# Optimization experiments

Hardware: AMD Instinct MI355X
Metric: run time of the kernel (lower is better)

The kernel has to match this reference:

```python
import jax, jax.numpy as jnp
import numpy as np

Q_MAX = 127.0  # int8 symmetric quantization range

def _ste_round(v):
    # straight-through round (matches quantize-forward semantics)
    return v + jax.lax.stop_gradient(jnp.round(v) - v)

def setup_inputs() -> dict:
    key = jax.random.key(0)
    k1, k2, k3, k4 = jax.random.split(key, 4)
    B, S, D_IN, D_OUT = 32, 577, 1024, 2560
    x = jax.random.normal(k1, (B, S, D_IN), dtype=jnp.float32)
    # pre-quantized int8 weight stored as int32 for jax friendliness
    w_int = jax.random.randint(k2, (D_OUT, D_IN), -127, 128, dtype=jnp.int32)
    # per-output-row dequant scales (absmax/127 style, small positive)
    scale_w = jax.random.uniform(k3, (D_OUT,), dtype=jnp.float32, minval=0.005, maxval=0.02)
    bias = jax.random.normal(k4, (D_OUT,), dtype=jnp.float32)
    return {"x": x, "w_int": w_int, "scale_w": scale_w, "bias": bias}

def reference(x, w_int, scale_w, bias):
    # bnb Int8Linear: dynamic per-row int8 quantization of activations,
    # per-column (output-feature) weight scales, then bias add.
    # x: [B, S, D_in], w_int: [D_out, D_in] in [-127,127], scale_w: [D_out]
    absmax_x = jnp.max(jnp.abs(x), axis=-1, keepdims=True)  # [B, S, 1]
    scale_x = jnp.maximum(absmax_x, 1e-8) / Q_MAX
    x_q = _ste_round(x / scale_x)  # quantized activations in [-127, 127]
    # integer-valued GEMM carried in fp32 accumulation
    acc = jnp.einsum("bsd,od->bso", x_q, w_int.astype(jnp.float32))
    y = acc * scale_x * scale_w[None, None, :] + bias[None, None, :]
    return y
```

## Files before the change

### kernel.cpp

```cpp
#include <hip/hip_runtime.h>
#include <stdint.h>

typedef int v4i __attribute__((ext_vector_type(4)));

__device__ __forceinline__ void gll16(const void* g, void* l) {
    __builtin_amdgcn_global_load_lds(
        (const __attribute__((address_space(1))) void*)(uintptr_t)g,
        (__attribute__((address_space(3))) void*)(uint32_t)(uintptr_t)l,
        16, 0, 0);
}

__global__ __launch_bounds__(256) void quant_x(const float* __restrict__ x,
                                               signed char* __restrict__ xq,
                                               float* __restrict__ sx, int M) {
    const int row = blockIdx.x;
    const int tid = threadIdx.x;
    signed char* qrow = xq + (size_t)row * 1024;
    if (row >= M) {
        ((char4*)qrow)[tid] = make_char4(0, 0, 0, 0);
        if (tid == 0) sx[row] = 0.0f;
        return;
    }
    const float4 v = ((const float4*)(x + (size_t)row * 1024))[tid];
    float a = fmaxf(fmaxf(fabsf(v.x), fabsf(v.y)), fmaxf(fabsf(v.z), fabsf(v.w)));
#pragma unroll
    for (int off = 32; off > 0; off >>= 1)
        a = fmaxf(a, __shfl_xor(a, off));
    __shared__ float red[4];
    if ((tid & 63) == 0) red[tid >> 6] = a;
    __syncthreads();
    const float am = fmaxf(fmaxf(red[0], red[1]), fmaxf(red[2], red[3]));
    const float amc = fmaxf(am, 1e-8f);
    const float scale = amc * (1.0f / 127.0f);
    const float inv = 127.0f / amc;
    char4 q;
    q.x = (signed char)(int)rintf(v.x * inv);
    q.y = (signed char)(int)rintf(v.y * inv);
    q.z = (signed char)(int)rintf(v.z * inv);
    q.w = (signed char)(int)rintf(v.w * inv);
    ((char4*)qrow)[tid] = q;
    if (tid == 0) sx[row] = scale;
}

__global__ __launch_bounds__(256) void conv_w(const int* __restrict__ w,
                                              signed char* __restrict__ w8, int n4) {
    const int i = blockIdx.x * 256 + threadIdx.x;
    if (i < n4) {
        const int4 v = ((const int4*)w)[i];
        char4 c;
        c.x = (signed char)v.x; c.y = (signed char)v.y;
        c.z = (signed char)v.z; c.w = (signed char)v.w;
        ((char4*)w8)[i] = c;
    }
}

__global__ __launch_bounds__(256) void gemm_i8(const signed char* __restrict__ xq,
                                               const signed char* __restrict__ w8,
                                               const float* __restrict__ sx,
                                               const float* __restrict__ sw,
                                               const float* __restrict__ bias,
                                               float* __restrict__ out,
                                               int M, int N, int K) {
    __shared__ signed char As[128 * 64];
    __shared__ signed char Bs[128 * 64];

    const int tid  = threadIdx.x;
    const int lane = tid & 63;
    const int wave = tid >> 6;
    const int wm = (wave & 1) * 64;
    const int wn = (wave >> 1) * 64;
    const int m_block = blockIdx.y * 128;
    const int n_block = blockIdx.x * 128;

    v4i acc[4][4];
#pragma unroll
    for (int mt = 0; mt < 4; ++mt)
#pragma unroll
        for (int nt = 0; nt < 4; ++nt) {
            acc[mt][nt].x = 0; acc[mt][nt].y = 0; acc[mt][nt].z = 0; acc[mt][nt].w = 0;
        }

    const int sr = tid >> 2;
    const int sc = ((tid & 3) ^ ((sr >> 1) & 3)) * 16;
    const signed char* aG = xq + (size_t)(m_block + sr) * K + sc;
    const signed char* bG = w8 + (size_t)(n_block + sr) * K + sc;
    signed char* aL = As + wave * 1024;
    signed char* bL = Bs + wave * 1024;

    const int fr  = lane & 15;
    const int fcs = (((lane >> 4) ^ ((lane >> 1) & 3))) * 16;

    for (int k0 = 0; k0 < K; k0 += 64) {
        if (k0) __syncthreads();
        gll16(aG + k0, aL);
        gll16(aG + k0 + (size_t)64 * K, aL + 4096);
        gll16(bG + k0, bL);
        gll16(bG + k0 + (size_t)64 * K, bL + 4096);
        __syncthreads();

        v4i af[4], bf[4];
#pragma unroll
        for (int mt = 0; mt < 4; ++mt)
            af[mt] = *(const v4i*)&As[(wm + mt * 16 + fr) * 64 + fcs];
#pragma unroll
        for (int nt = 0; nt < 4; ++nt)
            bf[nt] = *(const v4i*)&Bs[(wn + nt * 16 + fr) * 64 + fcs];
#pragma unroll
        for (int mt = 0; mt < 4; ++mt)
#pragma unroll
            for (int nt = 0; nt < 4; ++nt)
                acc[mt][nt] = __builtin_amdgcn_mfma_i32_16x16x64_i8(af[mt], bf[nt], acc[mt][nt], 0, 0, 0);
    }

    const int lr = lane >> 4;
    const int lc = lane & 15;
#pragma unroll
    for (int mt = 0; mt < 4; ++mt) {
        const int rbase = m_block + wm + mt * 16 + lr * 4;
        float sxv[4];
#pragma unroll
        for (int r = 0; r < 4; ++r)
            sxv[r] = (rbase + r < M) ? sx[rbase + r] : 0.0f;
#pragma unroll
        for (int nt = 0; nt < 4; ++nt) {
            const int col = n_block + wn + nt * 16 + lc;
            const float swv = sw[col];
            const float bv  = bias[col];
            const int* a = (const int*)&acc[mt][nt];
#pragma unroll
            for (int r = 0; r < 4; ++r) {
                const int row = rbase + r;
                if (row < M)
                    out[(size_t)row * N + col] = (float)a[r] * sxv[r] * swv + bv;
            }
        }
    }
}

extern "C" void kernel_launch(void* const* d_in, const int* in_sizes, int n_in,
                              void* d_out, int out_size, void* d_ws, size_t ws_size,
                              hipStream_t stream) {
    const float* x       = (const float*)d_in[0];
    const int*   w_int   = (const int*)d_in[1];
    const float* scale_w = (const float*)d_in[2];
    const float* bias    = (const float*)d_in[3];
    float* out = (float*)d_out;

    const int D_OUT = in_sizes[2];
    const int D_IN  = in_sizes[1] / D_OUT;
    const int M     = in_sizes[0] / D_IN;
    const int Mpad  = ((M + 127) / 128) * 128;

    signed char* xq = (signed char*)d_ws;
    signed char* w8 = xq + (size_t)Mpad * D_IN;
    float*       sx = (float*)(w8 + (size_t)D_OUT * D_IN);

    quant_x<<<Mpad, 256, 0, stream>>>(x, xq, sx, M);
    const int n4 = D_OUT * D_IN / 4;
    conv_w<<<(n4 + 255) / 256, 256, 0, stream>>>(w_int, w8, n4);
    dim3 grid(D_OUT / 128, Mpad / 128);
    gemm_i8<<<grid, dim3(256, 1, 1), 0, stream>>>(xq, w8, sx, scale_w, bias, out, M, D_OUT, D_IN);
}
```

Before: 317.5 us.

## Use 32x32x32 int8 MFMA with 128-deep K tiles and fuse prep kernels

Switches the GEMM inner loop from 16x16x64 to 32x32x32 int8 MFMA instructions, doubling the K-tile to 128 with a matching 8-way XOR swizzle in LDS. This means fewer barriers per K and better operand reuse per fragment load. The weight conversion and activation quantization kernels are merged into one launch to drop a kernel launch. The cost is twice the LDS per block (32 KB), which may reduce occupancy, and a 16-element accumulator epilogue with strided row stores.

```diff
diff --git a/kernel.cpp b/kernel.cpp
--- a/kernel.cpp
+++ b/kernel.cpp
@@ -1,7 +1,8 @@
 #include <hip/hip_runtime.h>
 #include <stdint.h>
 
-typedef int v4i __attribute__((ext_vector_type(4)));
+typedef int v4i  __attribute__((ext_vector_type(4)));
+typedef int v16i __attribute__((ext_vector_type(16)));
 
 __device__ __forceinline__ void gll16(const void* g, void* l) {
     __builtin_amdgcn_global_load_lds(
@@ -10,18 +11,30 @@
         16, 0, 0);
 }
 
-__global__ __launch_bounds__(256) void quant_x(const float* __restrict__ x,
-                                               signed char* __restrict__ xq,
-                                               float* __restrict__ sx, int M) {
-    const int row = blockIdx.x;
+__global__ __launch_bounds__(256) void prep(const float* __restrict__ x,
+                                            const int* __restrict__ w,
+                                            signed char* __restrict__ xq,
+                                            signed char* __restrict__ w8,
+                                            float* __restrict__ sx,
+                                            int M, int Mpad) {
+    const int b = blockIdx.x;
     const int tid = threadIdx.x;
-    signed char* qrow = xq + (size_t)row * 1024;
-    if (row >= M) {
-        ((char4*)qrow)[tid] = make_char4(0, 0, 0, 0);
-        if (tid == 0) sx[row] = 0.0f;
+    if (b >= Mpad) {
+        const int r = b - Mpad;
+        const int4 v = ((const int4*)(w + (size_t)r * 1024))[tid];
+        char4 c;
+        c.x = (signed char)v.x; c.y = (signed char)v.y;
+        c.z = (signed char)v.z; c.w = (signed char)v.w;
+        ((char4*)(w8 + (size_t)r * 1024))[tid] = c;
         return;
     }
-    const float4 v = ((const float4*)(x + (size_t)row * 1024))[tid];
+    signed char* qrow = xq + (size_t)b * 1024;
+    if (b >= M) {
+        ((char4*)qrow)[tid] = make_char4(0, 0, 0, 0);
+        if (tid == 0) sx[b] = 0.0f;
+        return;
+    }
+    const float4 v = ((const float4*)(x + (size_t)b * 1024))[tid];
     float a = fmaxf(fmaxf(fabsf(v.x), fabsf(v.y)), fmaxf(fabsf(v.z), fabsf(v.w)));
 #pragma unroll
     for (int off = 32; off > 0; off >>= 1)
@@ -31,7 +44,6 @@
     __syncthreads();
     const float am = fmaxf(fmaxf(red[0], red[1]), fmaxf(red[2], red[3]));
     const float amc = fmaxf(am, 1e-8f);
-    const float scale = amc * (1.0f / 127.0f);
     const float inv = 127.0f / amc;
     char4 q;
     q.x = (signed char)(int)rintf(v.x * inv);
@@ -39,19 +51,7 @@
     q.z = (signed char)(int)rintf(v.z * inv);
     q.w = (signed char)(int)rintf(v.w * inv);
     ((char4*)qrow)[tid] = q;
-    if (tid == 0) sx[row] = scale;
-}
-
-__global__ __launch_bounds__(256) void conv_w(const int* __restrict__ w,
-                                              signed char* __restrict__ w8, int n4) {
-    const int i = blockIdx.x * 256 + threadIdx.x;
-    if (i < n4) {
-        const int4 v = ((const int4*)w)[i];
-        char4 c;
-        c.x = (signed char)v.x; c.y = (signed char)v.y;
-        c.z = (signed char)v.z; c.w = (signed char)v.w;
-        ((char4*)w8)[i] = c;
-    }
+    if (tid == 0) sx[b] = amc * (1.0f / 127.0f);
 }
 
 __global__ __launch_bounds__(256) void gemm_i8(const signed char* __restrict__ xq,
@@ -61,8 +61,8 @@
                                                const float* __restrict__ bias,
                                                float* __restrict__ out,
                                                int M, int N, int K) {
-    __shared__ signed char As[128 * 64];
-    __shared__ signed char Bs[128 * 64];
+    __shared__ signed char As[128 * 128];
+    __shared__ signed char Bs[128 * 128];
 
     const int tid  = threadIdx.x;
     const int lane = tid & 63;
@@ -72,66 +72,75 @@
     const int m_block = blockIdx.y * 128;
     const int n_block = blockIdx.x * 128;
 
-    v4i acc[4][4];
+    v16i acc[2][2];
 #pragma unroll
-    for (int mt = 0; mt < 4; ++mt)
+    for (int mt = 0; mt < 2; ++mt)
 #pragma unroll
-        for (int nt = 0; nt < 4; ++nt) {
-            acc[mt][nt].x = 0; acc[mt][nt].y = 0; acc[mt][nt].z = 0; acc[mt][nt].w = 0;
-        }
+        for (int nt = 0; nt < 2; ++nt)
+#pragma unroll
+            for (int r = 0; r < 16; ++r)
+                acc[mt][nt][r] = 0;
 
-    const int sr = tid >> 2;
-    const int sc = ((tid & 3) ^ ((sr >> 1) & 3)) * 16;
-    const signed char* aG = xq + (size_t)(m_block + sr) * K + sc;
-    const signed char* bG = w8 + (size_t)(n_block + sr) * K + sc;
+    const int trow   = tid >> 3;
+    const int tchunk = ((tid & 7) ^ (trow & 7)) * 16;
+    const signed char* aG = xq + (size_t)(m_block + trow) * K + tchunk;
+    const signed char* bG = w8 + (size_t)(n_block + trow) * K + tchunk;
+    const size_t rowstep = (size_t)32 * K;
     signed char* aL = As + wave * 1024;
     signed char* bL = Bs + wave * 1024;
 
-    const int fr  = lane & 15;
-    const int fcs = (((lane >> 4) ^ ((lane >> 1) & 3))) * 16;
+    const int fr = lane & 31;
+    const int fk = lane >> 5;
+    const int fx = lane & 7;
 
-    for (int k0 = 0; k0 < K; k0 += 64) {
+    for (int k0 = 0; k0 < K; k0 += 128) {
         if (k0) __syncthreads();
-        gll16(aG + k0, aL);
-        gll16(aG + k0 + (size_t)64 * K, aL + 4096);
-        gll16(bG + k0, bL);
-        gll16(bG + k0 + (size_t)64 * K, bL + 4096);
+#pragma unroll
+        for (int i = 0; i < 4; ++i) {
+            gll16(aG + k0 + i * rowstep, aL + i * 4096);
+            gll16(bG + k0 + i * rowstep, bL + i * 4096);
+        }
         __syncthreads();
 
-        v4i af[4], bf[4];
 #pragma unroll
-        for (int mt = 0; mt < 4; ++mt)
-            af[mt] = *(const v4i*)&As[(wm + mt * 16 + fr) * 64 + fcs];
+        for (int kk = 0; kk < 4; ++kk) {
+            const int coff = ((kk * 2 + fk) ^ fx) * 16;
+            v4i af[2], bf[2];
 #pragma unroll
-        for (int nt = 0; nt < 4; ++nt)
-            bf[nt] = *(const v4i*)&Bs[(wn + nt * 16 + fr) * 64 + fcs];
+            for (int mt = 0; mt < 2; ++mt)
+                af[mt] = *(const v4i*)&As[(wm + mt * 32 + fr) * 128 + coff];
 #pragma unroll
-        for (int mt = 0; mt < 4; ++mt)
+            for (int nt = 0; nt < 2; ++nt)
+                bf[nt] = *(const v4i*)&Bs[(wn + nt * 32 + fr) * 128 + coff];
 #pragma unroll
-            for (int nt = 0; nt < 4; ++nt)
-                acc[mt][nt] = __builtin_amdgcn_mfma_i32_16x16x64_i8(af[mt], bf[nt], acc[mt][nt], 0, 0, 0);
+            for (int mt = 0; mt < 2; ++mt)
+#pragma unroll
+                for (int nt = 0; nt < 2; ++nt)
+                    acc[mt][nt] = __builtin_amdgcn_mfma_i32_32x32x32_i8(af[mt], bf[nt], acc[mt][nt], 0, 0, 0);
+        }
     }
 
-    const int lr = lane >> 4;
-    const int lc = lane & 15;
+    const int lc = lane & 31;
+    const int lh = (lane >> 5) * 4;
 #pragma unroll
-    for (int mt = 0; mt < 4; ++mt) {
-        const int rbase = m_block + wm + mt * 16 + lr * 4;
-        float sxv[4];
+    for (int mt = 0; mt < 2; ++mt) {
+        const int rbase = m_block + wm + mt * 32 + lh;
+        float sxv[16];
 #pragma unroll
-        for (int r = 0; r < 4; ++r)
-            sxv[r] = (rbase + r < M) ? sx[rbase + r] : 0.0f;
+        for (int r = 0; r < 16; ++r) {
+            const int row = rbase + (r & 3) + 8 * (r >> 2);
+            sxv[r] = (row < M) ? sx[row] : 0.0f;
+        }
 #pragma unroll
-        for (int nt = 0; nt < 4; ++nt) {
-            const int col = n_block + wn + nt * 16 + lc;
-            const float swv = sw[col];
+        for (int nt = 0; nt < 2; ++nt) {
+            const int col = n_block + wn + nt * 32 + lc;
+            const float sww = sw[col];
             const float bv  = bias[col];
-            const int* a = (const int*)&acc[mt][nt];
 #pragma unroll
-            for (int r = 0; r < 4; ++r) {
-                const int row = rbase + r;
+            for (int r = 0; r < 16; ++r) {
+                const int row = rbase + (r & 3) + 8 * (r >> 2);
                 if (row < M)
-                    out[(size_t)row * N + col] = (float)a[r] * sxv[r] * swv + bv;
+                    out[(size_t)row * N + col] = (float)acc[mt][nt][r] * sxv[r] * sww + bv;
             }
         }
     }
@@ -155,9 +164,7 @@
     signed char* w8 = xq + (size_t)Mpad * D_IN;
     float*       sx = (float*)(w8 + (size_t)D_OUT * D_IN);
 
-    quant_x<<<Mpad, 256, 0, stream>>>(x, xq, sx, M);
-    const int n4 = D_OUT * D_IN / 4;
-    conv_w<<<(n4 + 255) / 256, 256, 0, stream>>>(w_int, w8, n4);
+    prep<<<Mpad + D_OUT, 256, 0, stream>>>(x, w_int, xq, w8, sx, M, Mpad);
     dim3 grid(D_OUT / 128, Mpad / 128);
     gemm_i8<<<grid, dim3(256, 1, 1), 0, stream>>>(xq, w8, sx, scale_w, bias, out, M, D_OUT, D_IN);
 }
```

Measured after the change: 338.0 us. +6.5%, slower.

## Pre-pack int8 operands into MFMA fragment layout and load directly from global

Applied to the files above, without the earlier changes.

The activation-quantize and weight-convert kernels are merged into one prep kernel. It writes both int8 operands in a packed layout where each 16-row by 64-k fragment is contiguous, one 16-byte vector per lane. The GEMM then drops LDS staging and barriers and reads MFMA fragments straight from global memory with coalesced 16-byte loads, unrolled over k. This removes LDS traffic and sync overhead, but the kernel now depends on L2/cache hit rates for operand reuse across waves and blocks, and global-load latency is no longer hidden by shared-memory staging.

```diff
diff --git a/kernel.cpp b/kernel.cpp
--- a/kernel.cpp
+++ b/kernel.cpp
@@ -3,67 +3,90 @@
 
 typedef int v4i __attribute__((ext_vector_type(4)));
 
-__device__ __forceinline__ void gll16(const void* g, void* l) {
-    __builtin_amdgcn_global_load_lds(
-        (const __attribute__((address_space(1))) void*)(uintptr_t)g,
-        (__attribute__((address_space(3))) void*)(uint32_t)(uintptr_t)l,
-        16, 0, 0);
-}
+__global__ __launch_bounds__(256) void prep(const float* __restrict__ x,
+                                            const int* __restrict__ w,
+                                            signed char* __restrict__ xqp,
+                                            signed char* __restrict__ w8p,
+                                            float* __restrict__ sx,
+                                            int M, int MGpad) {
+    const int b = blockIdx.x;
+    const int t = threadIdx.x;
+    const int r = t >> 4;
+    const int s = t & 15;
 
-__global__ __launch_bounds__(256) void quant_x(const float* __restrict__ x,
-                                               signed char* __restrict__ xq,
-                                               float* __restrict__ sx, int M) {
-    const int row = blockIdx.x;
-    const int tid = threadIdx.x;
-    signed char* qrow = xq + (size_t)row * 1024;
-    if (row >= M) {
-        ((char4*)qrow)[tid] = make_char4(0, 0, 0, 0);
-        if (tid == 0) sx[row] = 0.0f;
+    if (b >= MGpad) {
+        const int g = b - MGpad;
+        const int row = g * 16 + r;
+        const int4* src = (const int4*)(w + (size_t)row * 1024 + s * 64);
+        signed char* dst = w8p + (((size_t)(g * 16 + s)) << 10) + r * 16;
+        int4 v[16];
+#pragma unroll
+        for (int i = 0; i < 16; ++i) v[i] = src[i];
+#pragma unroll
+        for (int c = 0; c < 4; ++c) {
+            int4 u;
+            uint32_t wds[4];
+#pragma unroll
+            for (int q = 0; q < 4; ++q) {
+                const int4 e = v[c * 4 + q];
+                wds[q] = ((uint32_t)(uint8_t)(signed char)e.x) |
+                         ((uint32_t)(uint8_t)(signed char)e.y << 8) |
+                         ((uint32_t)(uint8_t)(signed char)e.z << 16) |
+                         ((uint32_t)(uint8_t)(signed char)e.w << 24);
+            }
+            u.x = wds[0]; u.y = wds[1]; u.z = wds[2]; u.w = wds[3];
+            *(int4*)(dst + c * 256) = u;
+        }
         return;
     }
-    const float4 v = ((const float4*)(x + (size_t)row * 1024))[tid];
-    float a = fmaxf(fmaxf(fabsf(v.x), fabsf(v.y)), fmaxf(fabsf(v.z), fabsf(v.w)));
+
+    const int row = b * 16 + r;
+    float4 f[16];
+    if (row < M) {
+        const float4* src = (const float4*)(x + (size_t)row * 1024 + s * 64);
 #pragma unroll
-    for (int off = 32; off > 0; off >>= 1)
-        a = fmaxf(a, __shfl_xor(a, off));
-    __shared__ float red[4];
-    if ((tid & 63) == 0) red[tid >> 6] = a;
-    __syncthreads();
-    const float am = fmaxf(fmaxf(red[0], red[1]), fmaxf(red[2], red[3]));
+        for (int i = 0; i < 16; ++i) f[i] = src[i];
+    } else {
+#pragma unroll
+        for (int i = 0; i < 16; ++i) f[i] = make_float4(0.f, 0.f, 0.f, 0.f);
+    }
+    float am = 0.0f;
+#pragma unroll
+    for (int i = 0; i < 16; ++i)
+        am = fmaxf(am, fmaxf(fmaxf(fabsf(f[i].x), fabsf(f[i].y)),
+                             fmaxf(fabsf(f[i].z), fabsf(f[i].w))));
+#pragma unroll
+    for (int off = 1; off < 16; off <<= 1)
+        am = fmaxf(am, __shfl_xor(am, off));
     const float amc = fmaxf(am, 1e-8f);
-    const float scale = amc * (1.0f / 127.0f);
     const float inv = 127.0f / amc;
-    char4 q;
-    q.x = (signed char)(int)rintf(v.x * inv);
-    q.y = (signed char)(int)rintf(v.y * inv);
-    q.z = (signed char)(int)rintf(v.z * inv);
-    q.w = (signed char)(int)rintf(v.w * inv);
-    ((char4*)qrow)[tid] = q;
-    if (tid == 0) sx[row] = scale;
-}
+    if (s == 0) sx[row] = amc * (1.0f / 127.0f);
 
-__global__ __launch_bounds__(256) void conv_w(const int* __restrict__ w,
-                                              signed char* __restrict__ w8, int n4) {
-    const int i = blockIdx.x * 256 + threadIdx.x;
-    if (i < n4) {
-        const int4 v = ((const int4*)w)[i];
-        char4 c;
-        c.x = (signed char)v.x; c.y = (signed char)v.y;
-        c.z = (signed char)v.z; c.w = (signed char)v.w;
-        ((char4*)w8)[i] = c;
+    signed char* dst = xqp + (((size_t)(b * 16 + s)) << 10) + r * 16;
+#pragma unroll
+    for (int c = 0; c < 4; ++c) {
+        int4 u;
+        uint32_t wds[4];
+#pragma unroll
+        for (int q = 0; q < 4; ++q) {
+            const float4 e = f[c * 4 + q];
+            wds[q] = ((uint32_t)(uint8_t)(signed char)(int)rintf(e.x * inv)) |
+                     ((uint32_t)(uint8_t)(signed char)(int)rintf(e.y * inv) << 8) |
+                     ((uint32_t)(uint8_t)(signed char)(int)rintf(e.z * inv) << 16) |
+                     ((uint32_t)(uint8_t)(signed char)(int)rintf(e.w * inv) << 24);
+        }
+        u.x = wds[0]; u.y = wds[1]; u.z = wds[2]; u.w = wds[3];
+        *(int4*)(dst + c * 256) = u;
     }
 }
 
-__global__ __launch_bounds__(256) void gemm_i8(const signed char* __restrict__ xq,
-                                               const signed char* __restrict__ w8,
-                                               const float* __restrict__ sx,
-                                               const float* __restrict__ sw,
-                                               const float* __restrict__ bias,
-                                               float* __restrict__ out,
-                                               int M, int N, int K) {
-    __shared__ signed char As[128 * 64];
-    __shared__ signed char Bs[128 * 64];
-
+__global__ __launch_bounds__(256, 3) void gemm_i8(const signed char* __restrict__ ap,
+                                                  const signed char* __restrict__ bp,
+                                                  const float* __restrict__ sx,
+                                                  const float* __restrict__ sw,
+                                                  const float* __restrict__ bias,
+                                                  float* __restrict__ out,
+                                                  int M, int N, int KB) {
     const int tid  = threadIdx.x;
     const int lane = tid & 63;
     const int wave = tid >> 6;
@@ -71,6 +94,9 @@
     const int wn = (wave >> 1) * 64;
     const int m_block = blockIdx.y * 128;
     const int n_block = blockIdx.x * 128;
+
+    const signed char* aBase = ap + (((size_t)((m_block + wm) >> 4)) << 14) + lane * 16;
+    const signed char* bBase = bp + (((size_t)((n_block + wn) >> 4)) << 14) + lane * 16;
 
     v4i acc[4][4];
 #pragma unroll
@@ -80,31 +106,15 @@
             acc[mt][nt].x = 0; acc[mt][nt].y = 0; acc[mt][nt].z = 0; acc[mt][nt].w = 0;
         }
 
-    const int sr = tid >> 2;
-    const int sc = ((tid & 3) ^ ((sr >> 1) & 3)) * 16;
-    const signed char* aG = xq + (size_t)(m_block + sr) * K + sc;
-    const signed char* bG = w8 + (size_t)(n_block + sr) * K + sc;
-    signed char* aL = As + wave * 1024;
-    signed char* bL = Bs + wave * 1024;
-
-    const int fr  = lane & 15;
-    const int fcs = (((lane >> 4) ^ ((lane >> 1) & 3))) * 16;
-
-    for (int k0 = 0; k0 < K; k0 += 64) {
-        if (k0) __syncthreads();
-        gll16(aG + k0, aL);
-        gll16(aG + k0 + (size_t)64 * K, aL + 4096);
-        gll16(bG + k0, bL);
-        gll16(bG + k0 + (size_t)64 * K, bL + 4096);
-        __syncthreads();
-
+#pragma unroll 16
+    for (int kb = 0; kb < KB; ++kb) {
         v4i af[4], bf[4];
 #pragma unroll
         for (int mt = 0; mt < 4; ++mt)
-            af[mt] = *(const v4i*)&As[(wm + mt * 16 + fr) * 64 + fcs];
+            af[mt] = *(const v4i*)(aBase + (size_t)mt * 16384 + (size_t)kb * 1024);
 #pragma unroll
         for (int nt = 0; nt < 4; ++nt)
-            bf[nt] = *(const v4i*)&Bs[(wn + nt * 16 + fr) * 64 + fcs];
+            bf[nt] = *(const v4i*)(bBase + (size_t)nt * 16384 + (size_t)kb * 1024);
 #pragma unroll
         for (int mt = 0; mt < 4; ++mt)
 #pragma unroll
@@ -150,14 +160,15 @@
     const int D_IN  = in_sizes[1] / D_OUT;
     const int M     = in_sizes[0] / D_IN;
     const int Mpad  = ((M + 127) / 128) * 128;
+    const int MGpad = Mpad / 16;
+    const int NG    = D_OUT / 16;
+    const int KB    = D_IN / 64;
 
-    signed char* xq = (signed char*)d_ws;
-    signed char* w8 = xq + (size_t)Mpad * D_IN;
-    float*       sx = (float*)(w8 + (size_t)D_OUT * D_IN);
+    signed char* xqp = (signed char*)d_ws;
+    signed char* w8p = xqp + (size_t)Mpad * D_IN;
+    float*       sx  = (float*)(w8p + (size_t)D_OUT * D_IN);
 
-    quant_x<<<Mpad, 256, 0, stream>>>(x, xq, sx, M);
-    const int n4 = D_OUT * D_IN / 4;
-    conv_w<<<(n4 + 255) / 256, 256, 0, stream>>>(w_int, w8, n4);
+    prep<<<MGpad + NG, 256, 0, stream>>>(x, w_int, xqp, w8p, sx, M, MGpad);
     dim3 grid(D_OUT / 128, Mpad / 128);
-    gemm_i8<<<grid, dim3(256, 1, 1), 0, stream>>>(xq, w8, sx, scale_w, bias, out, M, D_OUT, D_IN);
+    gemm_i8<<<grid, dim3(256, 1, 1), 0, stream>>>(xqp, w8p, sx, scale_w, bias, out, M, D_OUT, KB);
 }
```

Result: slower. 325.0 us (+2.4%).
